# Performance work log

Measured on AMD Instinct MI355X. Metric: run time of the kernel, lower is better.

Reference implementation:

```python
import jax, jax.numpy as jnp
import numpy as np

N_LAYERS = 6
D_MODEL = 512
D_FFN = 2048
N_STATE = 64
KSIZE = 31
BATCH = 8
SEQ = 2048
IN_SIZE = 80


def _ln(x, g, b, eps=1e-5):
    m = jnp.mean(x, axis=-1, keepdims=True)
    v = jnp.mean((x - m) ** 2, axis=-1, keepdims=True)
    return (x - m) * jax.lax.rsqrt(v + eps) * g + b


def _ffn(x, g, b, w1, b1, w2, b2):
    # LayerNorm -> Linear(D->F) -> GELU -> Linear(F->D)  (PositionalwiseFeedForward)
    h = jax.nn.gelu(_ln(x, g, b) @ w1 + b1)
    return h @ w2 + b2


def _dss(x, lam_re, lam_im, c_re, c_im, d_skip, log_dt, w_out, b_out):
    # Diagonal state-space (DSS-EXP): generate length-T kernel from diagonal poles,
    # apply causal conv via FFT, skip D*u, GELU, GLU output projection.
    Bx, T, H = x.shape
    dt = jnp.exp(log_dt)
    lam = -jnp.exp(lam_re) + 1j * lam_im                        # [N] stable poles (Re<0)
    P = jnp.exp(lam[:, None] * (dt * jnp.arange(T))[None, :])   # [N, T]
    C = c_re + 1j * c_im                                        # [H, N]
    kern = jnp.einsum('hn,nt->ht', C, P).real * dt              # [H, T]
    u = x.transpose(0, 2, 1)                                    # [B, H, T]
    n = 2 * T
    y = jnp.fft.irfft(jnp.fft.rfft(u, n=n) * jnp.fft.rfft(kern, n=n), n=n)[..., :T]
    y = y + d_skip[None, :, None] * u
    y = jax.nn.gelu(y.transpose(0, 2, 1))                       # [B, T, H]
    z = y @ w_out + b_out                                       # [B, T, 2H]
    a, g = jnp.split(z, 2, axis=-1)
    return a * jax.nn.sigmoid(g)                                # GLU


def _conv_module(x, g1, b1, bw, bb, dw, db, g2, b2, lw, lb):
    # LN -> 1x1 conv to 2D + GLU -> depthwise conv (SAME, k=31) -> LN -> GELU -> Linear
    y = _ln(x, g1, b1)
    y = y @ bw.T + bb                                           # [B, T, 2D]
    a, g = jnp.split(y, 2, axis=-1)
    y = a * jax.nn.sigmoid(g)                                   # GLU over channels
    yc = y.transpose(0, 2, 1)                                   # [B, D, T]
    yc = jax.lax.conv_general_dilated(
        yc, dw[:, None, :], (1,), 'SAME',
        feature_group_count=yc.shape[1],
        dimension_numbers=('NCH', 'OIH', 'NCH'))
    yc = yc + db[None, :, None]
    y = jax.nn.gelu(_ln(yc.transpose(0, 2, 1), g2, b2))
    return y @ lw.T + lb


def _forward(src, speaker_embs, src_w, src_b,
             ffn1_ln_g, ffn1_ln_b, ffn1_w1, ffn1_b1, ffn1_w2, ffn1_b2,
             norm1_g, norm1_b,
             lam_re, lam_im, c_re, c_im, ssm_d, log_dt, dss_out_w, dss_out_b,
             conv_ln_g, conv_ln_b, bneck_w, bneck_b, dw_w, dw_b,
             conv_ln2_g, conv_ln2_b, conv_lin_w, conv_lin_b,
             ffn2_ln_g, ffn2_ln_b, ffn2_w1, ffn2_b1, ffn2_w2, ffn2_b2,
             norm2_g, norm2_b, final_g, final_b):
    x = src @ src_w + src_b                                     # custom_src_module Linear
    for i in range(N_LAYERS):
        x = x + 0.5 * _ffn(x, ffn1_ln_g[i], ffn1_ln_b[i], ffn1_w1[i], ffn1_b1[i], ffn1_w2[i], ffn1_b2[i])
        skip = x
        x = _ln(x, norm1_g[i], norm1_b[i])
        x = _dss(x, lam_re[i], lam_im[i], c_re[i], c_im[i], ssm_d[i], log_dt[i], dss_out_w[i], dss_out_b[i])
        x = x + skip
        x = x + _conv_module(x, conv_ln_g[i], conv_ln_b[i], bneck_w[i], bneck_b[i], dw_w[i], dw_b[i],
                             conv_ln2_g[i], conv_ln2_b[i], conv_lin_w[i], conv_lin_b[i])
        x = _ln(x + 0.5 * _ffn(x, ffn2_ln_g[i], ffn2_ln_b[i], ffn2_w1[i], ffn2_b1[i], ffn2_w2[i], ffn2_b2[i]),
                norm2_g[i], norm2_b[i])
    x = _ln(x, final_g, final_b, eps=1e-6)
    return x + speaker_embs


def setup_inputs() -> dict:
    key = jax.random.key(0)
    ks = iter(jax.random.split(key, 64))
    def rn(shape, s=0.02):
        return (jax.random.normal(next(ks), shape) * s).astype(jnp.float32)
    L, D, F, N, K = N_LAYERS, D_MODEL, D_FFN, N_STATE, KSIZE
    return dict(
        src=jax.random.normal(next(ks), (BATCH, SEQ, IN_SIZE), dtype=jnp.float32),
        speaker_embs=jax.random.normal(next(ks), (BATCH, 1, D), dtype=jnp.float32),
        src_w=rn((IN_SIZE, D)), src_b=jnp.zeros((D,), jnp.float32),
        ffn1_ln_g=jnp.ones((L, D), jnp.float32), ffn1_ln_b=jnp.zeros((L, D), jnp.float32),
        ffn1_w1=rn((L, D, F)), ffn1_b1=jnp.zeros((L, F), jnp.float32),
        ffn1_w2=rn((L, F, D)), ffn1_b2=jnp.zeros((L, D), jnp.float32),
        norm1_g=jnp.ones((L, D), jnp.float32), norm1_b=jnp.zeros((L, D), jnp.float32),
        lam_re=rn((L, N), 0.5), lam_im=rn((L, N), 3.0),
        c_re=rn((L, D, N), 0.1), c_im=rn((L, D, N), 0.1),
        ssm_d=rn((L, D), 1.0), log_dt=jnp.full((L,), float(np.log(0.01)), jnp.float32),
        dss_out_w=rn((L, D, 2 * D)), dss_out_b=jnp.zeros((L, 2 * D), jnp.float32),
        conv_ln_g=jnp.ones((L, D), jnp.float32), conv_ln_b=jnp.zeros((L, D), jnp.float32),
        bneck_w=rn((L, 2 * D, D)), bneck_b=jnp.zeros((L, 2 * D), jnp.float32),
        dw_w=rn((L, D, K), 0.1), dw_b=jnp.zeros((L, D), jnp.float32),
        conv_ln2_g=jnp.ones((L, D), jnp.float32), conv_ln2_b=jnp.zeros((L, D), jnp.float32),
        conv_lin_w=rn((L, D, D)), conv_lin_b=jnp.zeros((L, D), jnp.float32),
        ffn2_ln_g=jnp.ones((L, D), jnp.float32), ffn2_ln_b=jnp.zeros((L, D), jnp.float32),
        ffn2_w1=rn((L, D, F)), ffn2_b1=jnp.zeros((L, F), jnp.float32),
        ffn2_w2=rn((L, F, D)), ffn2_b2=jnp.zeros((L, D), jnp.float32),
        norm2_g=jnp.ones((L, D), jnp.float32), norm2_b=jnp.zeros((L, D), jnp.float32),
        final_g=jnp.ones((D,), jnp.float32), final_b=jnp.zeros((D,), jnp.float32),
    )


def reference(src, speaker_embs, src_w, src_b,
              ffn1_ln_g, ffn1_ln_b, ffn1_w1, ffn1_b1, ffn1_w2, ffn1_b2,
              norm1_g, norm1_b,
              lam_re, lam_im, c_re, c_im, ssm_d, log_dt, dss_out_w, dss_out_b,
              conv_ln_g, conv_ln_b, bneck_w, bneck_b, dw_w, dw_b,
              conv_ln2_g, conv_ln2_b, conv_lin_w, conv_lin_b,
              ffn2_ln_g, ffn2_ln_b, ffn2_w1, ffn2_b1, ffn2_w2, ffn2_b2,
              norm2_g, norm2_b, final_g, final_b):
    return _forward(src, speaker_embs, src_w, src_b,
                    ffn1_ln_g, ffn1_ln_b, ffn1_w1, ffn1_b1, ffn1_w2, ffn1_b2,
                    norm1_g, norm1_b,
                    lam_re, lam_im, c_re, c_im, ssm_d, log_dt, dss_out_w, dss_out_b,
                    conv_ln_g, conv_ln_b, bneck_w, bneck_b, dw_w, dw_b,
                    conv_ln2_g, conv_ln2_b, conv_lin_w, conv_lin_b,
                    ffn2_ln_g, ffn2_ln_b, ffn2_w1, ffn2_b1, ffn2_w2, ffn2_b2,
                    norm2_g, norm2_b, final_g, final_b)
```

## Files before the change

### kernel.cpp

```cpp
#include <hip/hip_runtime.h>
#include <hip/hip_bf16.h>
#include <stdint.h>


#define NL 6
#define TT 2048
#define BB 8
#define DD 512
#define FF 2048
#define ROWS (BB*TT)

typedef __attribute__((ext_vector_type(4))) float f32x4;
typedef __attribute__((ext_vector_type(8))) short s16x8;

#define DEVI __device__ __forceinline__

DEVI float bf2f(uint32_t u) { union { uint32_t i; float f; } v; v.i = u << 16; return v.f; }
DEVI uint16_t f2bf(float f) {
    union { float f; uint32_t i; } v; v.f = f;
    uint32_t x = v.i;
    return (uint16_t)((x + 0x7fffu + ((x >> 16) & 1u)) >> 16);
}
DEVI float gelu_f(float x) {
    float x3 = x * x * x;
    float a  = 0.7978845608028654f * (x + 0.044715f * x3);
    float e  = __expf(2.0f * a);
    float t  = 1.0f - 2.0f / (e + 1.0f);
    return 0.5f * x * (1.0f + t);
}
DEVI float sigm(float x) { return 1.0f / (1.0f + __expf(-x)); }

__global__ void k_wtrans(const float* __restrict__ src, uint16_t* __restrict__ dst,
                         int K, int N) {
    __shared__ float tile[32][33];
    int l = blockIdx.z;
    const float* s = src + (size_t)l * K * N;
    uint16_t*    d = dst + (size_t)l * N * K;
    int n0 = blockIdx.x * 32, k0 = blockIdx.y * 32;
    int tx = threadIdx.x, ty = threadIdx.y;
#pragma unroll
    for (int i = 0; i < 4; i++) {
        int k = k0 + ty + i * 8;
        tile[ty + i * 8][tx] = s[(size_t)k * N + n0 + tx];
    }
    __syncthreads();
#pragma unroll
    for (int i = 0; i < 4; i++) {
        int n = n0 + ty + i * 8;
        d[(size_t)n * K + k0 + tx] = f2bf(tile[tx][ty + i * 8]);
    }
}
__global__ void k_wcvt(const float* __restrict__ src, uint16_t* __restrict__ dst, int n) {
    int i = blockIdx.x * 256 + threadIdx.x;
    if (i < n) dst[i] = f2bf(src[i]);
}
__global__ void k_dwt(const float* __restrict__ dw, float* __restrict__ dwt) {
    int i = blockIdx.x * 256 + threadIdx.x;
    int tot = NL * DD * 31;
    if (i >= tot) return;
    int l = i / (DD * 31), r = i % (DD * 31), d = r / 31, k = r % 31;
    dwt[(size_t)l * 31 * DD + k * DD + d] = dw[i];
}

__global__ void k_inproj(const float* __restrict__ src, const float* __restrict__ W,
                         const float* __restrict__ bias, float* __restrict__ X) {
    __shared__ float srow[80];
    int r = blockIdx.x, tid = threadIdx.x;
    if (tid < 80) srow[tid] = src[(size_t)r * 80 + tid];
    __syncthreads();
    int c = tid * 2;
    float a0 = bias[c], a1 = bias[c + 1];
    for (int k = 0; k < 80; k++) {
        float s = srow[k];
        const float2 w = *(const float2*)(W + (size_t)k * DD + c);
        a0 = fmaf(s, w.x, a0);
        a1 = fmaf(s, w.y, a1);
    }
    float2* px = (float2*)(X + (size_t)r * DD + c);
    *px = make_float2(a0, a1);
}

template <int MODE>
__global__ void k_ln(const float* __restrict__ in, void* __restrict__ outp,
                     const float* __restrict__ gam, const float* __restrict__ bet,
                     const float* __restrict__ spk, float eps) {
    int row  = blockIdx.x * 4 + (threadIdx.x >> 6);
    int lane = threadIdx.x & 63;
    const float* x = in + (size_t)row * DD;
    float4 a0 = *(const float4*)&x[lane * 4];
    float4 a1 = *(const float4*)&x[256 + lane * 4];
    float v[8] = {a0.x, a0.y, a0.z, a0.w, a1.x, a1.y, a1.z, a1.w};
    float s = 0.f, q = 0.f;
#pragma unroll
    for (int i = 0; i < 8; i++) { s += v[i]; q += v[i] * v[i]; }
#pragma unroll
    for (int m = 1; m < 64; m <<= 1) { s += __shfl_xor(s, m); q += __shfl_xor(q, m); }
    float mean = s * (1.0f / 512.0f);
    float var  = fmaxf(q * (1.0f / 512.0f) - mean * mean, 0.0f);
    float inv  = rsqrtf(var + eps);
    float4 g0 = *(const float4*)&gam[lane * 4];
    float4 g1 = *(const float4*)&gam[256 + lane * 4];
    float4 b0 = *(const float4*)&bet[lane * 4];
    float4 b1 = *(const float4*)&bet[256 + lane * 4];
    float gv[8] = {g0.x, g0.y, g0.z, g0.w, g1.x, g1.y, g1.z, g1.w};
    float bv[8] = {b0.x, b0.y, b0.z, b0.w, b1.x, b1.y, b1.z, b1.w};
    float y[8];
#pragma unroll
    for (int i = 0; i < 8; i++) y[i] = (v[i] - mean) * inv * gv[i] + bv[i];
    if (MODE == 1) {
#pragma unroll
        for (int i = 0; i < 8; i++) y[i] = gelu_f(y[i]);
    }
    if (MODE == 0 || MODE == 1) {
        uint16_t* o = (uint16_t*)outp + (size_t)row * DD;
        uint2 p0, p1;
        p0.x = (uint32_t)f2bf(y[0]) | ((uint32_t)f2bf(y[1]) << 16);
        p0.y = (uint32_t)f2bf(y[2]) | ((uint32_t)f2bf(y[3]) << 16);
        p1.x = (uint32_t)f2bf(y[4]) | ((uint32_t)f2bf(y[5]) << 16);
        p1.y = (uint32_t)f2bf(y[6]) | ((uint32_t)f2bf(y[7]) << 16);
        *(uint2*)&o[lane * 4]       = p0;
        *(uint2*)&o[256 + lane * 4] = p1;
    } else {
        float* o = (float*)outp + (size_t)row * DD;
        if (MODE == 3) {
            const float* sp = spk + (size_t)(row >> 11) * DD;
            float4 s0 = *(const float4*)&sp[lane * 4];
            float4 s1 = *(const float4*)&sp[256 + lane * 4];
            y[0] += s0.x; y[1] += s0.y; y[2] += s0.z; y[3] += s0.w;
            y[4] += s1.x; y[5] += s1.y; y[6] += s1.z; y[7] += s1.w;
        }
        *(float4*)&o[lane * 4]       = make_float4(y[0], y[1], y[2], y[3]);
        *(float4*)&o[256 + lane * 4] = make_float4(y[4], y[5], y[6], y[7]);
    }
}

template <int MODE>
__global__ __launch_bounds__(256) void k_gemm(
    const uint16_t* __restrict__ A, const uint16_t* __restrict__ Bt,
    const float* __restrict__ bias, int M, int N, int K,
    void* __restrict__ outp, float* __restrict__ X) {
    __shared__ __align__(16) uint16_t As[128 * 40];
    __shared__ __align__(16) uint16_t Bs[128 * 40];
    int tid = threadIdx.x;
    int m0 = blockIdx.x * 128, n0 = blockIdx.y * 128;
    int wave = tid >> 6, lane = tid & 63;
    int wm = (wave >> 1) * 64, wn = (wave & 1) * 64;
    int l15 = lane & 15, l16 = lane >> 4;

    f32x4 acc[4][4];
#pragma unroll
    for (int i = 0; i < 4; i++)
#pragma unroll
        for (int j = 0; j < 4; j++) acc[i][j] = (f32x4){0.f, 0.f, 0.f, 0.f};

    for (int kt = 0; kt < K; kt += 32) {
#pragma unroll
        for (int i = 0; i < 2; i++) {
            int idx = tid + i * 256;
            int row = idx >> 2, kq = idx & 3;
            uint4 va = *(const uint4*)(A  + (size_t)(m0 + row) * K + kt + kq * 8);
            *(uint4*)&As[row * 40 + kq * 8] = va;
            uint4 vb = *(const uint4*)(Bt + (size_t)(n0 + row) * K + kt + kq * 8);
            *(uint4*)&Bs[row * 40 + kq * 8] = vb;
        }
        __syncthreads();
        s16x8 af[4], bfr[4];
#pragma unroll
        for (int i = 0; i < 4; i++)
            af[i] = *(const s16x8*)&As[(wm + i * 16 + l15) * 40 + l16 * 8];
#pragma unroll
        for (int j = 0; j < 4; j++)
            bfr[j] = *(const s16x8*)&Bs[(wn + j * 16 + l15) * 40 + l16 * 8];
#pragma unroll
        for (int i = 0; i < 4; i++)
#pragma unroll
            for (int j = 0; j < 4; j++)
                acc[i][j] = __builtin_amdgcn_mfma_f32_16x16x32_bf16(af[i], bfr[j], acc[i][j], 0, 0, 0);
        __syncthreads();
    }
#pragma unroll
    for (int i = 0; i < 4; i++) {
#pragma unroll
        for (int j = 0; j < 4; j++) {
            int gcol = n0 + wn + j * 16 + l15;
            float bv = bias[gcol];
#pragma unroll
            for (int q = 0; q < 4; q++) {
                int grow = m0 + wm + i * 16 + l16 * 4 + q;
                float v = acc[i][j][q] + bv;
                if (MODE == 0) {
                    ((uint16_t*)outp)[(size_t)grow * N + gcol] = f2bf(gelu_f(v));
                } else if (MODE == 1) {
                    ((uint16_t*)outp)[(size_t)grow * N + gcol] = f2bf(v);
                } else if (MODE == 2) {
                    X[(size_t)grow * DD + gcol] += 0.5f * v;
                } else if (MODE == 3) {
                    X[(size_t)grow * DD + gcol] += v;
                } else {
                    ((float*)outp)[(size_t)grow * DD + gcol] =
                        X[(size_t)grow * DD + gcol] + 0.5f * v;
                }
            }
        }
    }
}

__global__ void k_tpose(const uint16_t* __restrict__ in, uint16_t* __restrict__ out,
                        int R, int C) {
    __shared__ uint16_t tile[32][33];
    size_t boff = (size_t)blockIdx.z * R * C;
    int c0 = blockIdx.x * 32, r0 = blockIdx.y * 32;
    int tx = threadIdx.x, ty = threadIdx.y;
#pragma unroll
    for (int i = 0; i < 4; i++)
        tile[ty + i * 8][tx] = in[boff + (size_t)(r0 + ty + i * 8) * C + c0 + tx];
    __syncthreads();
#pragma unroll
    for (int i = 0; i < 4; i++)
        out[boff + (size_t)(c0 + ty + i * 8) * R + r0 + tx] = tile[tx][ty + i * 8];
}


__global__ __launch_bounds__(64) void k_phiprep(
        const float* __restrict__ lam_re, const float* __restrict__ lam_im,
        const float* __restrict__ log_dt, uint16_t* __restrict__ PHI,
        float* __restrict__ A64f) {
    int l = blockIdx.x, n = threadIdx.x;
    float dt = expf(log_dt[l]);
    float lr = lam_re[l * 64 + n], li = lam_im[l * 64 + n];
    float mag = expf(-expf(lr) * dt), th = li * dt;
    float Are = mag * __cosf(th), Aim = mag * __sinf(th);
    float Pre = 1.f, Pim = 0.f;
    uint16_t* ph = PHI + (size_t)l * 8192;
    for (int tau = 0; tau < 64; tau++) {
        int s = 63 - tau;
        ph[n * 64 + s]        = f2bf(Pre);
        ph[(64 + n) * 64 + s] = f2bf(Pim);
        float nr = Pre * Are - Pim * Aim;
        float ni = Pre * Aim + Pim * Are;
        Pre = nr; Pim = ni;
    }
    A64f[l * 128 + 2 * n]     = Pre;
    A64f[l * 128 + 2 * n + 1] = Pim;
}

__global__ __launch_bounds__(64) void k_gprep(
        const float* __restrict__ lam_re, const float* __restrict__ lam_im,
        const float* __restrict__ c_re, const float* __restrict__ c_im,
        const float* __restrict__ ssm_d, const float* __restrict__ log_dt,
        int l, uint16_t* __restrict__ G) {
    int h = blockIdx.x, n = threadIdx.x;
    __shared__ float klds[64];
    float dt = expf(log_dt[l]);
    float lr = lam_re[l * 64 + n], li = lam_im[l * 64 + n];
    float mag = expf(-expf(lr) * dt), th = li * dt;
    float Are = mag * __cosf(th), Aim = mag * __sinf(th);
    float Cre = c_re[(size_t)l * DD * 64 + h * 64 + n];
    float Cim = c_im[(size_t)l * DD * 64 + h * 64 + n];
    uint16_t* Gh = G + (size_t)h * 64 * 192;
    float Pre = 1.f, Pim = 0.f;
    for (int r = 0; r < 64; r++) {
        float t = Cre * Pre - Cim * Pim;
        float s = t;
        s += __shfl_xor(s, 1);  s += __shfl_xor(s, 2);  s += __shfl_xor(s, 4);
        s += __shfl_xor(s, 8);  s += __shfl_xor(s, 16); s += __shfl_xor(s, 32);
        if (n == 0) klds[r] = dt * s;
        float nr = Pre * Are - Pim * Aim;
        float ni = Pre * Aim + Pim * Are;
        float wre = dt * (Cre * nr - Cim * ni);
        float wim = dt * (Cre * ni + Cim * nr);
        Gh[r * 192 + 64 + n]  = f2bf(wre);
        Gh[r * 192 + 128 + n] = f2bf(-wim);
        Pre = nr; Pim = ni;
    }
    __syncthreads();
    float dh = ssm_d[l * DD + h];
    for (int r = 0; r < 64; r++) {
        int c = n;
        float val = (c < r) ? klds[r - c] : (c == r ? klds[0] + dh : 0.f);
        Gh[r * 192 + c] = f2bf(val);
    }
}

__global__ __launch_bounds__(256) void k_pass1(
        const uint16_t* __restrict__ u, const uint16_t* __restrict__ PHI,
        uint16_t* __restrict__ E) {
    __shared__ __align__(16) uint16_t Phs[128 * 72];
    int tid = threadIdx.x;
    for (int v = tid; v < 1024; v += 256) {
        int row = v >> 3, kb = v & 7;
        *(s16x8*)&Phs[row * 72 + kb * 8] = *(const s16x8*)&PHI[row * 64 + kb * 8];
    }
    __syncthreads();
    int wave = tid >> 6, lane = tid & 63;
    int l15 = lane & 15, l16 = lane >> 4;
    int m0 = (wave & 1) * 64;
    int colbase = blockIdx.x * 128 + (wave >> 1) * 64;
    f32x4 acc[4][4];
#pragma unroll
    for (int i = 0; i < 4; i++)
#pragma unroll
        for (int j = 0; j < 4; j++) acc[i][j] = (f32x4){0.f, 0.f, 0.f, 0.f};
#pragma unroll
    for (int kt = 0; kt < 64; kt += 32) {
        s16x8 a[4], b[4];
#pragma unroll
        for (int i = 0; i < 4; i++)
            a[i] = *(const s16x8*)&Phs[(m0 + i * 16 + l15) * 72 + kt + l16 * 8];
#pragma unroll
        for (int j = 0; j < 4; j++)
            b[j] = *(const s16x8*)(u + (size_t)(colbase + j * 16 + l15) * 64 + kt + l16 * 8);
#pragma unroll
        for (int i = 0; i < 4; i++)
#pragma unroll
            for (int j = 0; j < 4; j++)
                acc[i][j] = __builtin_amdgcn_mfma_f32_16x16x32_bf16(a[i], b[j], acc[i][j], 0, 0, 0);
    }
#pragma unroll
    for (int i = 0; i < 4; i++)
#pragma unroll
        for (int j = 0; j < 4; j++) {
            int col = colbase + j * 16 + l15;
            int r0  = m0 + i * 16 + l16 * 4;
            uint32_t p0 = (uint32_t)f2bf(acc[i][j][0]) | ((uint32_t)f2bf(acc[i][j][1]) << 16);
            uint32_t p1 = (uint32_t)f2bf(acc[i][j][2]) | ((uint32_t)f2bf(acc[i][j][3]) << 16);
            *(uint2*)&E[(size_t)col * 128 + r0] = make_uint2(p0, p1);
        }
}

__global__ void k_pass2(const uint16_t* __restrict__ E, const float* __restrict__ A64f,
                        int l, uint16_t* __restrict__ Sp) {
    int gid = blockIdx.x * 256 + threadIdx.x;
    int n = gid & 63, bh = gid >> 6;
    int b = bh >> 9, h = bh & 511;
    float2 A = *(const float2*)&A64f[l * 128 + 2 * n];
    float Sre = 0.f, Sim = 0.f;
    const uint16_t* Eb = E + (size_t)bh * 32 * 128;
    uint16_t* So = Sp + (size_t)h * 32768 + (size_t)b * 32 * 128;
    for (int i = 0; i < 32; i++) {
        So[i * 128 + n]      = f2bf(Sre);
        So[i * 128 + 64 + n] = f2bf(Sim);
        float er = bf2f((uint32_t)Eb[i * 128 + n]);
        float ei = bf2f((uint32_t)Eb[i * 128 + 64 + n]);
        float nr = A.x * Sre - A.y * Sim + er;
        float ni = A.x * Sim + A.y * Sre + ei;
        Sre = nr; Sim = ni;
    }
}

__global__ __launch_bounds__(256) void k_pass3(
        const uint16_t* __restrict__ G, const uint16_t* __restrict__ u,
        const uint16_t* __restrict__ Sp, uint16_t* __restrict__ Y) {
    __shared__ __align__(16) uint16_t Gs[64 * 200];
    int h = blockIdx.x, tid = threadIdx.x;
    for (int v = tid; v < 1536; v += 256) {
        int row = v / 24, kb = v % 24;
        *(s16x8*)&Gs[row * 200 + kb * 8] = *(const s16x8*)&G[(size_t)h * 12288 + row * 192 + kb * 8];
    }
    __syncthreads();
    int wave = tid >> 6, lane = tid & 63;
    int l15 = lane & 15, l16 = lane >> 4;
    int wn = wave * 64;
    const uint16_t* uh = u + (size_t)h * TT;
    const uint16_t* sh = Sp + (size_t)h * 32768;
    f32x4 acc[4][4];
#pragma unroll
    for (int i = 0; i < 4; i++)
#pragma unroll
        for (int j = 0; j < 4; j++) acc[i][j] = (f32x4){0.f, 0.f, 0.f, 0.f};
#pragma unroll
    for (int kt = 0; kt < 192; kt += 32) {
        s16x8 a[4], b[4];
#pragma unroll
        for (int i = 0; i < 4; i++)
            a[i] = *(const s16x8*)&Gs[(i * 16 + l15) * 200 + kt + l16 * 8];
#pragma unroll
        for (int j = 0; j < 4; j++) {
            int col = wn + j * 16 + l15;
            const uint16_t* src;
            if (kt < 64)
                src = uh + (size_t)(col >> 5) * (DD * TT) + (col & 31) * 64 + kt + l16 * 8;
            else
                src = sh + (size_t)col * 128 + (kt - 64) + l16 * 8;
            b[j] = *(const s16x8*)src;
        }
#pragma unroll
        for (int i = 0; i < 4; i++)
#pragma unroll
            for (int j = 0; j < 4; j++)
                acc[i][j] = __builtin_amdgcn_mfma_f32_16x16x32_bf16(a[i], b[j], acc[i][j], 0, 0, 0);
    }
#pragma unroll
    for (int i = 0; i < 4; i++)
#pragma unroll
        for (int j = 0; j < 4; j++) {
            int col = wn + j * 16 + l15;
            int r0  = i * 16 + l16 * 4;
            uint16_t* dst = Y + (size_t)(col >> 5) * (DD * TT) + (size_t)h * TT + (col & 31) * 64 + r0;
            uint32_t p0 = (uint32_t)f2bf(acc[i][j][0]) | ((uint32_t)f2bf(acc[i][j][1]) << 16);
            uint32_t p1 = (uint32_t)f2bf(acc[i][j][2]) | ((uint32_t)f2bf(acc[i][j][3]) << 16);
            *(uint2*)&dst[0] = make_uint2(p0, p1);
        }
}

__global__ void k_tgelu(const uint16_t* __restrict__ y, uint16_t* __restrict__ out) {
    __shared__ uint16_t tile[32][33];
    int b = blockIdx.z;
    int t0 = blockIdx.x * 32, h0 = blockIdx.y * 32;
    int tx = threadIdx.x, ty = threadIdx.y;
    const uint16_t* yb = y + (size_t)b * DD * TT;
#pragma unroll
    for (int i = 0; i < 4; i++) {
        int h = h0 + ty + i * 8;
        tile[ty + i * 8][tx] = f2bf(gelu_f(bf2f((uint32_t)yb[(size_t)h * TT + t0 + tx])));
    }
    __syncthreads();
    uint16_t* ob = out + (size_t)b * TT * DD;
#pragma unroll
    for (int i = 0; i < 4; i++) {
        int t = t0 + ty + i * 8;
        ob[(size_t)t * DD + h0 + tx] = tile[tx][ty + i * 8];
    }
}

template <int SKIP>
__global__ void k_glu(const uint16_t* __restrict__ z, float* __restrict__ X,
                      uint16_t* __restrict__ out) {
    int i = blockIdx.x * 256 + threadIdx.x;
    int r = i >> 8;
    int c = (i & 255) * 2;
    uint32_t av = *(const uint32_t*)&z[(size_t)r * 1024 + c];
    uint32_t gv = *(const uint32_t*)&z[(size_t)r * 1024 + 512 + c];
    float a0 = bf2f(av & 0xffffu), a1 = bf2f(av >> 16);
    float g0 = bf2f(gv & 0xffffu), g1 = bf2f(gv >> 16);
    float v0 = a0 * sigm(g0), v1 = a1 * sigm(g1);
    if (SKIP) {
        float2* px = (float2*)&X[(size_t)r * DD + c];
        float2 x = *px;
        x.x += v0; x.y += v1;
        *px = x;
    } else {
        uint32_t p = (uint32_t)f2bf(v0) | ((uint32_t)f2bf(v1) << 16);
        *(uint32_t*)&out[(size_t)r * DD + c] = p;
    }
}

__global__ void k_dwconv(const uint16_t* __restrict__ in, const float* __restrict__ dwt,
                         const float* __restrict__ db, float* __restrict__ out) {
    int i = blockIdx.x * 256 + threadIdx.x;
    int d = (i & 255) * 2;
    int t = (i >> 8) & (TT - 1);
    int b = i >> 19;
    float a0 = db[d], a1 = db[d + 1];
    const uint16_t* ib = in + (size_t)b * TT * DD;
#pragma unroll
    for (int j = 0; j < 31; j++) {
        int tj = t + j - 15;
        if (tj >= 0 && tj < TT) {
            uint32_t v = *(const uint32_t*)&ib[(size_t)tj * DD + d];
            float2 w = *(const float2*)&dwt[j * DD + d];
            a0 = fmaf(bf2f(v & 0xffffu), w.x, a0);
            a1 = fmaf(bf2f(v >> 16), w.y, a1);
        }
    }
    size_t off = ((size_t)b * TT + t) * DD + d;
    *(float2*)&out[off] = make_float2(a0, a1);
}

extern "C" void kernel_launch(void* const* d_in, const int* in_sizes, int n_in,
                              void* d_out, int out_size, void* d_ws, size_t ws_size,
                              hipStream_t stream) {
    const float* src        = (const float*)d_in[0];
    const float* speaker    = (const float*)d_in[1];
    const float* src_w      = (const float*)d_in[2];
    const float* src_b      = (const float*)d_in[3];
    const float* ffn1_ln_g  = (const float*)d_in[4];
    const float* ffn1_ln_b  = (const float*)d_in[5];
    const float* ffn1_w1    = (const float*)d_in[6];
    const float* ffn1_b1    = (const float*)d_in[7];
    const float* ffn1_w2    = (const float*)d_in[8];
    const float* ffn1_b2    = (const float*)d_in[9];
    const float* norm1_g    = (const float*)d_in[10];
    const float* norm1_b    = (const float*)d_in[11];
    const float* lam_re     = (const float*)d_in[12];
    const float* lam_im     = (const float*)d_in[13];
    const float* c_re       = (const float*)d_in[14];
    const float* c_im       = (const float*)d_in[15];
    const float* ssm_d      = (const float*)d_in[16];
    const float* log_dt     = (const float*)d_in[17];
    const float* dss_out_w  = (const float*)d_in[18];
    const float* dss_out_b  = (const float*)d_in[19];
    const float* conv_ln_g  = (const float*)d_in[20];
    const float* conv_ln_b  = (const float*)d_in[21];
    const float* bneck_w    = (const float*)d_in[22];
    const float* bneck_b    = (const float*)d_in[23];
    const float* dw_w       = (const float*)d_in[24];
    const float* dw_b       = (const float*)d_in[25];
    const float* conv_ln2_g = (const float*)d_in[26];
    const float* conv_ln2_b = (const float*)d_in[27];
    const float* conv_lin_w = (const float*)d_in[28];
    const float* conv_lin_b = (const float*)d_in[29];
    const float* ffn2_ln_g  = (const float*)d_in[30];
    const float* ffn2_ln_b  = (const float*)d_in[31];
    const float* ffn2_w1    = (const float*)d_in[32];
    const float* ffn2_b1    = (const float*)d_in[33];
    const float* ffn2_w2    = (const float*)d_in[34];
    const float* ffn2_b2    = (const float*)d_in[35];
    const float* norm2_g    = (const float*)d_in[36];
    const float* norm2_b    = (const float*)d_in[37];
    const float* final_g    = (const float*)d_in[38];
    const float* final_b    = (const float*)d_in[39];
    (void)in_sizes; (void)n_in; (void)out_size; (void)ws_size;

    uint8_t* ws = (uint8_t*)d_ws;
    float*    X   = (float*)   (ws + 0);
    float*    F0  = (float*)   (ws + 33554432);
    uint16_t* B1  = (uint16_t*)(ws + 67108864);
    uint16_t* B2  = (uint16_t*)(ws + 83886080);
    uint16_t* B3  = (uint16_t*)(ws + 100663296);
    uint16_t* H   = (uint16_t*)(ws + 117440512);
    uint16_t* Wf1a= (uint16_t*)(ws + 184549376);
    uint16_t* Wf1b= (uint16_t*)(ws + 197132288);
    uint16_t* Wds = (uint16_t*)(ws + 209715200);
    uint16_t* Wbn = (uint16_t*)(ws + 216006656);
    uint16_t* Wcl = (uint16_t*)(ws + 222298112);
    uint16_t* Wf2a= (uint16_t*)(ws + 225443840);
    uint16_t* Wf2b= (uint16_t*)(ws + 238026752);
    float*    DWT = (float*)   (ws + 250609664);
    uint16_t* PHI = (uint16_t*)(ws + 250990592);
    float*    A64f= (float*)   (ws + 251088896);

    uint16_t* GBUF = B1;
    uint16_t* SPK  = (uint16_t*)F0;
    uint16_t* EBUF = H;

    dim3 tb(32, 8);
    k_wtrans<<<dim3(FF/32, DD/32, NL), tb, 0, stream>>>(ffn1_w1, Wf1a, DD, FF);
    k_wtrans<<<dim3(DD/32, FF/32, NL), tb, 0, stream>>>(ffn1_w2, Wf1b, FF, DD);
    k_wtrans<<<dim3(1024/32, DD/32, NL), tb, 0, stream>>>(dss_out_w, Wds, DD, 1024);
    k_wcvt<<<(NL*1024*DD + 255)/256, 256, 0, stream>>>(bneck_w, Wbn, NL*1024*DD);
    k_wcvt<<<(NL*DD*DD + 255)/256, 256, 0, stream>>>(conv_lin_w, Wcl, NL*DD*DD);
    k_wtrans<<<dim3(FF/32, DD/32, NL), tb, 0, stream>>>(ffn2_w1, Wf2a, DD, FF);
    k_wtrans<<<dim3(DD/32, FF/32, NL), tb, 0, stream>>>(ffn2_w2, Wf2b, FF, DD);
    k_dwt<<<(NL*DD*31 + 255)/256, 256, 0, stream>>>(dw_w, DWT);
    k_phiprep<<<NL, 64, 0, stream>>>(lam_re, lam_im, log_dt, PHI, A64f);

    k_inproj<<<ROWS, 256, 0, stream>>>(src, src_w, src_b, X);

    for (int l = 0; l < NL; l++) {
        k_ln<0><<<4096, 256, 0, stream>>>(X, B1, ffn1_ln_g + l*DD, ffn1_ln_b + l*DD, nullptr, 1e-5f);
        k_gemm<0><<<dim3(128, 16), 256, 0, stream>>>(B1, Wf1a + (size_t)l*FF*DD, ffn1_b1 + l*FF,
                                                     ROWS, FF, DD, H, nullptr);
        k_gemm<2><<<dim3(128, 4), 256, 0, stream>>>(H, Wf1b + (size_t)l*DD*FF, ffn1_b2 + l*DD,
                                                    ROWS, DD, FF, nullptr, X);
        k_ln<0><<<4096, 256, 0, stream>>>(X, B1, norm1_g + l*DD, norm1_b + l*DD, nullptr, 1e-5f);
        k_tpose<<<dim3(DD/32, TT/32, BB), tb, 0, stream>>>(B1, B2, TT, DD);
        k_gprep<<<DD, 64, 0, stream>>>(lam_re, lam_im, c_re, c_im, ssm_d, log_dt, l, GBUF);
        k_pass1<<<1024, 256, 0, stream>>>(B2, PHI + (size_t)l*8192, EBUF);
        k_pass2<<<1024, 256, 0, stream>>>(EBUF, A64f, l, SPK);
        k_pass3<<<DD, 256, 0, stream>>>(GBUF, B2, SPK, B3);
        k_tgelu<<<dim3(TT/32, DD/32, BB), tb, 0, stream>>>(B3, B1);
        k_gemm<1><<<dim3(128, 8), 256, 0, stream>>>(B1, Wds + (size_t)l*1024*DD, dss_out_b + l*1024,
                                                    ROWS, 1024, DD, H, nullptr);
        k_glu<1><<<ROWS, 256, 0, stream>>>(H, X, nullptr);
        k_ln<0><<<4096, 256, 0, stream>>>(X, B1, conv_ln_g + l*DD, conv_ln_b + l*DD, nullptr, 1e-5f);
        k_gemm<1><<<dim3(128, 8), 256, 0, stream>>>(B1, Wbn + (size_t)l*1024*DD, bneck_b + l*1024,
                                                    ROWS, 1024, DD, H, nullptr);
        k_glu<0><<<ROWS, 256, 0, stream>>>(H, nullptr, B2);
        k_dwconv<<<ROWS, 256, 0, stream>>>(B2, DWT + (size_t)l*31*DD, dw_b + l*DD, F0);
        k_ln<1><<<4096, 256, 0, stream>>>(F0, B1, conv_ln2_g + l*DD, conv_ln2_b + l*DD, nullptr, 1e-5f);
        k_gemm<3><<<dim3(128, 4), 256, 0, stream>>>(B1, Wcl + (size_t)l*DD*DD, conv_lin_b + l*DD,
                                                    ROWS, DD, DD, nullptr, X);
        k_ln<0><<<4096, 256, 0, stream>>>(X, B1, ffn2_ln_g + l*DD, ffn2_ln_b + l*DD, nullptr, 1e-5f);
        k_gemm<0><<<dim3(128, 16), 256, 0, stream>>>(B1, Wf2a + (size_t)l*FF*DD, ffn2_b1 + l*FF,
                                                     ROWS, FF, DD, H, nullptr);
        k_gemm<4><<<dim3(128, 4), 256, 0, stream>>>(H, Wf2b + (size_t)l*DD*FF, ffn2_b2 + l*DD,
                                                    ROWS, DD, FF, F0, X);
        k_ln<2><<<4096, 256, 0, stream>>>(F0, X, norm2_g + l*DD, norm2_b + l*DD, nullptr, 1e-5f);
    }
    k_ln<3><<<4096, 256, 0, stream>>>(X, d_out, final_g, final_b, speaker, 1e-6f);
}
```

Baseline: 3.759 ms.

## Use direct global-to-LDS loads in GEMM, tile depthwise conv, GEMM input projection

The GEMM tile load now uses global_load_lds to write straight into shared memory in the MFMA fragment order, skipping the register round trip and the padded layout. The depthwise conv stages a 34-row time window in LDS so each block computes 4 output timesteps and reuses loaded inputs. The input projection becomes a bf16 MFMA GEMM over padded K=96 instead of a scalar fp32 loop. Risks: the unpadded LDS layout may cause bank conflicts, and the input projection loses precision by running in bf16.

```diff
diff --git a/kernel.cpp b/kernel.cpp
--- a/kernel.cpp
+++ b/kernel.cpp
@@ -29,6 +29,11 @@
     return 0.5f * x * (1.0f + t);
 }
 DEVI float sigm(float x) { return 1.0f / (1.0f + __expf(-x)); }
+
+DEVI void gload16(const uint16_t* g, uint16_t* l) {
+    __builtin_amdgcn_global_load_lds((const __attribute__((address_space(1))) void*)g,
+                                     (__attribute__((address_space(3))) void*)l, 16, 0, 0);
+}
 
 __global__ void k_wtrans(const float* __restrict__ src, uint16_t* __restrict__ dst,
                          int K, int N) {
@@ -61,23 +66,17 @@
     int l = i / (DD * 31), r = i % (DD * 31), d = r / 31, k = r % 31;
     dwt[(size_t)l * 31 * DD + k * DD + d] = dw[i];
 }
-
-__global__ void k_inproj(const float* __restrict__ src, const float* __restrict__ W,
-                         const float* __restrict__ bias, float* __restrict__ X) {
-    __shared__ float srow[80];
-    int r = blockIdx.x, tid = threadIdx.x;
-    if (tid < 80) srow[tid] = src[(size_t)r * 80 + tid];
-    __syncthreads();
-    int c = tid * 2;
-    float a0 = bias[c], a1 = bias[c + 1];
-    for (int k = 0; k < 80; k++) {
-        float s = srow[k];
-        const float2 w = *(const float2*)(W + (size_t)k * DD + c);
-        a0 = fmaf(s, w.x, a0);
-        a1 = fmaf(s, w.y, a1);
-    }
-    float2* px = (float2*)(X + (size_t)r * DD + c);
-    *px = make_float2(a0, a1);
+__global__ void k_srcpad(const float* __restrict__ src, uint16_t* __restrict__ dst) {
+    int i = blockIdx.x * 256 + threadIdx.x;
+    if (i >= ROWS * 96) return;
+    int r = i / 96, c = i - r * 96;
+    dst[i] = (c < 80) ? f2bf(src[(size_t)r * 80 + c]) : (uint16_t)0;
+}
+__global__ void k_wsrcpad(const float* __restrict__ w, uint16_t* __restrict__ dst) {
+    int i = blockIdx.x * 256 + threadIdx.x;
+    if (i >= DD * 96) return;
+    int n = i / 96, k = i - n * 96;
+    dst[i] = (k < 80) ? f2bf(w[(size_t)k * DD + n]) : (uint16_t)0;
 }
 
 template <int MODE>
@@ -139,14 +138,22 @@
     const uint16_t* __restrict__ A, const uint16_t* __restrict__ Bt,
     const float* __restrict__ bias, int M, int N, int K,
     void* __restrict__ outp, float* __restrict__ X) {
-    __shared__ __align__(16) uint16_t As[128 * 40];
-    __shared__ __align__(16) uint16_t Bs[128 * 40];
+    __shared__ __align__(16) uint16_t As[128 * 32];
+    __shared__ __align__(16) uint16_t Bs[128 * 32];
     int tid = threadIdx.x;
     int m0 = blockIdx.x * 128, n0 = blockIdx.y * 128;
     int wave = tid >> 6, lane = tid & 63;
     int wm = (wave >> 1) * 64, wn = (wave & 1) * 64;
     int l15 = lane & 15, l16 = lane >> 4;
 
+    const uint16_t* gA = A  + (size_t)(m0 + 32 * wave + l15) * K + l16 * 8;
+    const uint16_t* gB = Bt + (size_t)(n0 + 32 * wave + l15) * K + l16 * 8;
+    uint16_t* lA0 = &As[(2 * wave) * 512];
+    uint16_t* lA1 = &As[(2 * wave + 1) * 512];
+    uint16_t* lB0 = &Bs[(2 * wave) * 512];
+    uint16_t* lB1 = &Bs[(2 * wave + 1) * 512];
+    size_t rowskip = (size_t)16 * K;
+
     f32x4 acc[4][4];
 #pragma unroll
     for (int i = 0; i < 4; i++)
@@ -154,23 +161,18 @@
         for (int j = 0; j < 4; j++) acc[i][j] = (f32x4){0.f, 0.f, 0.f, 0.f};
 
     for (int kt = 0; kt < K; kt += 32) {
-#pragma unroll
-        for (int i = 0; i < 2; i++) {
-            int idx = tid + i * 256;
-            int row = idx >> 2, kq = idx & 3;
-            uint4 va = *(const uint4*)(A  + (size_t)(m0 + row) * K + kt + kq * 8);
-            *(uint4*)&As[row * 40 + kq * 8] = va;
-            uint4 vb = *(const uint4*)(Bt + (size_t)(n0 + row) * K + kt + kq * 8);
-            *(uint4*)&Bs[row * 40 + kq * 8] = vb;
-        }
+        gload16(gA + kt, lA0);
+        gload16(gA + rowskip + kt, lA1);
+        gload16(gB + kt, lB0);
+        gload16(gB + rowskip + kt, lB1);
         __syncthreads();
         s16x8 af[4], bfr[4];
 #pragma unroll
         for (int i = 0; i < 4; i++)
-            af[i] = *(const s16x8*)&As[(wm + i * 16 + l15) * 40 + l16 * 8];
+            af[i] = *(const s16x8*)&As[((wave >> 1) * 4 + i) * 512 + lane * 8];
 #pragma unroll
         for (int j = 0; j < 4; j++)
-            bfr[j] = *(const s16x8*)&Bs[(wn + j * 16 + l15) * 40 + l16 * 8];
+            bfr[j] = *(const s16x8*)&Bs[((wave & 1) * 4 + j) * 512 + lane * 8];
 #pragma unroll
         for (int i = 0; i < 4; i++)
 #pragma unroll
@@ -196,9 +198,11 @@
                     X[(size_t)grow * DD + gcol] += 0.5f * v;
                 } else if (MODE == 3) {
                     X[(size_t)grow * DD + gcol] += v;
-                } else {
+                } else if (MODE == 4) {
                     ((float*)outp)[(size_t)grow * DD + gcol] =
                         X[(size_t)grow * DD + gcol] + 0.5f * v;
+                } else {
+                    X[(size_t)grow * DD + gcol] = v;
                 }
             }
         }
@@ -445,26 +449,41 @@
     }
 }
 
-__global__ void k_dwconv(const uint16_t* __restrict__ in, const float* __restrict__ dwt,
-                         const float* __restrict__ db, float* __restrict__ out) {
-    int i = blockIdx.x * 256 + threadIdx.x;
-    int d = (i & 255) * 2;
-    int t = (i >> 8) & (TT - 1);
-    int b = i >> 19;
-    float a0 = db[d], a1 = db[d + 1];
+__global__ __launch_bounds__(256) void k_dwconv(
+        const uint16_t* __restrict__ in, const float* __restrict__ dwt,
+        const float* __restrict__ db, float* __restrict__ out) {
+    __shared__ __align__(16) uint16_t xs[34 * 512];
+    int tid = threadIdx.x;
+    int t0 = (blockIdx.x & 511) * 4;
+    int b  = blockIdx.x >> 9;
     const uint16_t* ib = in + (size_t)b * TT * DD;
-#pragma unroll
-    for (int j = 0; j < 31; j++) {
-        int tj = t + j - 15;
-        if (tj >= 0 && tj < TT) {
-            uint32_t v = *(const uint32_t*)&ib[(size_t)tj * DD + d];
-            float2 w = *(const float2*)&dwt[j * DD + d];
-            a0 = fmaf(bf2f(v & 0xffffu), w.x, a0);
-            a1 = fmaf(bf2f(v >> 16), w.y, a1);
+    for (int v = tid; v < 34 * 64; v += 256) {
+        int row = v >> 6, seg = v & 63;
+        int tj = t0 - 15 + row;
+        uint4 val = make_uint4(0, 0, 0, 0);
+        if (tj >= 0 && tj < TT) val = *(const uint4*)&ib[(size_t)tj * DD + seg * 8];
+        *(uint4*)&xs[row * 512 + seg * 8] = val;
+    }
+    __syncthreads();
+    int d = tid * 2;
+    float a0[4], a1[4];
+    float bv0 = db[d], bv1 = db[d + 1];
+#pragma unroll
+    for (int o = 0; o < 4; o++) { a0[o] = bv0; a1[o] = bv1; }
+#pragma unroll
+    for (int k = 0; k < 31; k++) {
+        float2 w = *(const float2*)&dwt[k * DD + d];
+#pragma unroll
+        for (int o = 0; o < 4; o++) {
+            uint32_t v = *(const uint32_t*)&xs[(o + k) * 512 + d];
+            a0[o] = fmaf(bf2f(v & 0xffffu), w.x, a0[o]);
+            a1[o] = fmaf(bf2f(v >> 16), w.y, a1[o]);
         }
     }
-    size_t off = ((size_t)b * TT + t) * DD + d;
-    *(float2*)&out[off] = make_float2(a0, a1);
+#pragma unroll
+    for (int o = 0; o < 4; o++) {
+        *(float2*)&out[((size_t)b * TT + t0 + o) * DD + d] = make_float2(a0[o], a1[o]);
+    }
 }
 
 extern "C" void kernel_launch(void* const* d_in, const int* in_sizes, int n_in,
@@ -533,6 +552,8 @@
     uint16_t* GBUF = B1;
     uint16_t* SPK  = (uint16_t*)F0;
     uint16_t* EBUF = H;
+    uint16_t* SRCB = B3;
+    uint16_t* WSRC = B2;
 
     dim3 tb(32, 8);
     k_wtrans<<<dim3(FF/32, DD/32, NL), tb, 0, stream>>>(ffn1_w1, Wf1a, DD, FF);
@@ -544,8 +565,10 @@
     k_wtrans<<<dim3(DD/32, FF/32, NL), tb, 0, stream>>>(ffn2_w2, Wf2b, FF, DD);
     k_dwt<<<(NL*DD*31 + 255)/256, 256, 0, stream>>>(dw_w, DWT);
     k_phiprep<<<NL, 64, 0, stream>>>(lam_re, lam_im, log_dt, PHI, A64f);
-
-    k_inproj<<<ROWS, 256, 0, stream>>>(src, src_w, src_b, X);
+    k_srcpad<<<(ROWS*96 + 255)/256, 256, 0, stream>>>(src, SRCB);
+    k_wsrcpad<<<(DD*96 + 255)/256, 256, 0, stream>>>(src_w, WSRC);
+
+    k_gemm<5><<<dim3(128, 4), 256, 0, stream>>>(SRCB, WSRC, src_b, ROWS, DD, 96, nullptr, X);
 
     for (int l = 0; l < NL; l++) {
         k_ln<0><<<4096, 256, 0, stream>>>(X, B1, ffn1_ln_g + l*DD, ffn1_ln_b + l*DD, nullptr, 1e-5f);
@@ -567,7 +590,7 @@
         k_gemm<1><<<dim3(128, 8), 256, 0, stream>>>(B1, Wbn + (size_t)l*1024*DD, bneck_b + l*1024,
                                                     ROWS, 1024, DD, H, nullptr);
         k_glu<0><<<ROWS, 256, 0, stream>>>(H, nullptr, B2);
-        k_dwconv<<<ROWS, 256, 0, stream>>>(B2, DWT + (size_t)l*31*DD, dw_b + l*DD, F0);
+        k_dwconv<<<BB*512, 256, 0, stream>>>(B2, DWT + (size_t)l*31*DD, dw_b + l*DD, F0);
         k_ln<1><<<4096, 256, 0, stream>>>(F0, B1, conv_ln2_g + l*DD, conv_ln2_b + l*DD, nullptr, 1e-5f);
         k_gemm<3><<<dim3(128, 4), 256, 0, stream>>>(B1, Wcl + (size_t)l*DD*DD, conv_lin_b + l*DD,
                                                     ROWS, DD, DD, nullptr, X);
```

Measured after the change: 3.843 ms. +2.2%, slower.
